# Optimization experiments

Measured on AMD Instinct MI355X. Metric: run time of the kernel, lower is better.

The kernel has to match this reference:

```python
import jax, jax.numpy as jnp
import numpy as np

FACTOR = 8
IN_DIM = 4096
OUT_DIM = 4096


def setup_inputs() -> dict:
    key = jax.random.key(0)
    kx, ka, ks = jax.random.split(key, 3)
    x = jax.random.normal(kx, (4, 2048, IN_DIM), dtype=jnp.float32)
    a = jax.random.normal(ka, (FACTOR, FACTOR, FACTOR), dtype=jnp.float32) * 0.1
    s = jax.random.normal(ks, (FACTOR, OUT_DIM // FACTOR, IN_DIM // FACTOR), dtype=jnp.float32) * 0.05
    return {"x": x, "a": a, "s": s}


def reference(x, a, s):
    f = a.shape[0]
    out_dim = a.shape[1] * s.shape[1]
    in_dim = a.shape[2] * s.shape[2]
    # Batched Kronecker product: (f, a_rows*k, a_cols*p) then sum over batch dim f.
    # weight[a*k + ?, c*p + ?] = sum_b a[b, ar, ac] * s[b, kr, pc]
    p = jnp.einsum('bac,bkp->bakcp', a, s)  # (f, f, out/f, f, in/f)
    weight = p.reshape(f, out_dim, in_dim).sum(axis=0)  # (out, in)
    return x @ weight.T
```

## Files before the change

kernel.cpp:

```cpp
#include <hip/hip_runtime.h>
#include <hip/hip_bf16.h>
#include <stdint.h>

namespace {

constexpr int MTOT = 8192;
constexpr int NTOT = 4096;
constexpr int KTOT = 4096;

constexpr int BM = 256, BN = 256, BK = 32;
constexpr int NT = KTOT / BK;

typedef __attribute__((ext_vector_type(8))) short bf16x8;
typedef __attribute__((ext_vector_type(4))) float f32x4;

__device__ inline unsigned short to_bf16(float f) {
    union { float f; uint32_t u; } v; v.f = f;
    return (unsigned short)((v.u + 0x7FFFu + ((v.u >> 16) & 1u)) >> 16);
}

__global__ __launch_bounds__(256) void convert_x_kernel(const float* __restrict__ x,
                                                        unsigned short* __restrict__ xb) {
    int idx = blockIdx.x * 256 + threadIdx.x;
    const f32x4* xv = reinterpret_cast<const f32x4*>(x);
    f32x4 v0 = xv[2 * idx];
    f32x4 v1 = xv[2 * idx + 1];
    union { bf16x8 v; unsigned short s[8]; } o;
    o.s[0] = to_bf16(v0.x); o.s[1] = to_bf16(v0.y);
    o.s[2] = to_bf16(v0.z); o.s[3] = to_bf16(v0.w);
    o.s[4] = to_bf16(v1.x); o.s[5] = to_bf16(v1.y);
    o.s[6] = to_bf16(v1.z); o.s[7] = to_bf16(v1.w);
    reinterpret_cast<bf16x8*>(xb)[idx] = o.v;
}

__global__ __launch_bounds__(256) void gen_w_kernel(const float* __restrict__ a,
                                                    const float* __restrict__ s,
                                                    unsigned short* __restrict__ w) {
    int idx = blockIdx.x * 256 + threadIdx.x;
    int o  = idx >> 9;
    int i8 = idx & 511;
    int i0 = i8 * 8;
    int obig = o >> 9, orow = o & 511;
    int ibig = i0 >> 9, icol = i0 & 511;

    float acc[8];
#pragma unroll
    for (int j = 0; j < 8; ++j) acc[j] = 0.f;

#pragma unroll
    for (int b = 0; b < 8; ++b) {
        float av = a[b * 64 + obig * 8 + ibig];
        const f32x4* sv = reinterpret_cast<const f32x4*>(s + b * 512 * 512 + orow * 512 + icol);
        f32x4 s0 = sv[0], s1 = sv[1];
        acc[0] += av * s0.x; acc[1] += av * s0.y; acc[2] += av * s0.z; acc[3] += av * s0.w;
        acc[4] += av * s1.x; acc[5] += av * s1.y; acc[6] += av * s1.z; acc[7] += av * s1.w;
    }
    union { bf16x8 v; unsigned short q[8]; } ov;
#pragma unroll
    for (int j = 0; j < 8; ++j) ov.q[j] = to_bf16(acc[j]);
    reinterpret_cast<bf16x8*>(w)[idx] = ov.v;
}

__global__ __launch_bounds__(512, 2)
void gemm_bt_kernel(const unsigned short* __restrict__ A,
                    const unsigned short* __restrict__ B,
                    float* __restrict__ C) {
    __shared__ __align__(16) unsigned short As[4][BM][BK];
    __shared__ __align__(16) unsigned short Bs[4][BN][BK];

    int bid = blockIdx.x;
    int swz = (bid & 7) * 64 + (bid >> 3);
    int bm = swz >> 4;
    int bn = swz & 15;

    int tid  = threadIdx.x;
    int wid  = tid >> 6;
    int lane = tid & 63;
    int wm = wid >> 2, wn = wid & 3;

    int srow  = lane >> 2;
    int sslot = (lane & 3) ^ ((srow >> 1) & 3);
    const unsigned short* ag0 = A + (size_t)(bm * BM + wid * 16 + srow) * KTOT + sslot * 8;
    const unsigned short* ag1 = ag0 + (size_t)128 * KTOT;
    const unsigned short* bg0 = B + (size_t)(bn * BN + wid * 16 + srow) * KTOT + sslot * 8;
    const unsigned short* bg1 = bg0 + (size_t)128 * KTOT;

    int rl    = lane & 15;
    int rslot = (lane >> 4) ^ ((rl >> 1) & 3);

    f32x4 acc[8][4];
#pragma unroll
    for (int m = 0; m < 8; ++m)
#pragma unroll
        for (int n = 0; n < 4; ++n) acc[m][n] = (f32x4)0.f;

    auto STAGE = [&](int s, int k0) {
        __builtin_amdgcn_global_load_lds(
            (const __attribute__((address_space(1))) void*)(ag0 + k0),
            (__attribute__((address_space(3))) void*)&As[s][wid * 16][0], 16, 0, 0);
        __builtin_amdgcn_global_load_lds(
            (const __attribute__((address_space(1))) void*)(ag1 + k0),
            (__attribute__((address_space(3))) void*)&As[s][128 + wid * 16][0], 16, 0, 0);
        __builtin_amdgcn_global_load_lds(
            (const __attribute__((address_space(1))) void*)(bg0 + k0),
            (__attribute__((address_space(3))) void*)&Bs[s][wid * 16][0], 16, 0, 0);
        __builtin_amdgcn_global_load_lds(
            (const __attribute__((address_space(1))) void*)(bg1 + k0),
            (__attribute__((address_space(3))) void*)&Bs[s][128 + wid * 16][0], 16, 0, 0);
    };

    auto BODY = [&](int s) {
        bf16x8 af[8], bf[4];
#pragma unroll
        for (int m = 0; m < 8; ++m)
            af[m] = *reinterpret_cast<const bf16x8*>(&As[s][wm * 128 + m * 16 + rl][rslot * 8]);
#pragma unroll
        for (int n = 0; n < 4; ++n)
            bf[n] = *reinterpret_cast<const bf16x8*>(&Bs[s][wn * 64 + n * 16 + rl][rslot * 8]);
        __builtin_amdgcn_s_setprio(1);
#pragma unroll
        for (int m = 0; m < 8; ++m)
#pragma unroll
            for (int n = 0; n < 4; ++n)
                acc[m][n] = __builtin_amdgcn_mfma_f32_16x16x32_bf16(af[m], bf[n], acc[m][n], 0, 0, 0);
        __builtin_amdgcn_s_setprio(0);
    };

    STAGE(0, 0);
    STAGE(1, BK);
    STAGE(2, 2 * BK);
    asm volatile("s_waitcnt vmcnt(8)" ::: "memory");
    __builtin_amdgcn_s_barrier();
    __builtin_amdgcn_sched_barrier(0);

    for (int t = 0; t < NT - 3; ++t) {
        STAGE((t + 3) & 3, (t + 3) * BK);
        BODY(t & 3);
        asm volatile("s_waitcnt vmcnt(8)" ::: "memory");
        __builtin_amdgcn_s_barrier();
        __builtin_amdgcn_sched_barrier(0);
    }
    BODY((NT - 3) & 3);
    asm volatile("s_waitcnt vmcnt(4)" ::: "memory");
    __builtin_amdgcn_s_barrier();
    __builtin_amdgcn_sched_barrier(0);

    BODY((NT - 2) & 3);
    asm volatile("s_waitcnt vmcnt(0)" ::: "memory");
    __builtin_amdgcn_s_barrier();
    __builtin_amdgcn_sched_barrier(0);

    BODY((NT - 1) & 3);

    int crow0 = bm * BM + wm * 128 + (lane >> 4) * 4;
    int ccol0 = bn * BN + wn * 64 + (lane & 15);
#pragma unroll
    for (int m = 0; m < 8; ++m)
#pragma unroll
        for (int n = 0; n < 4; ++n)
#pragma unroll
            for (int j = 0; j < 4; ++j) {
                size_t r = (size_t)(crow0 + m * 16 + j);
                size_t c = (size_t)(ccol0 + n * 16);
                C[r * NTOT + c] = acc[m][n][j];
            }
}

}

extern "C" void kernel_launch(void* const* d_in, const int* in_sizes, int n_in,
                              void* d_out, int out_size, void* d_ws, size_t ws_size,
                              hipStream_t stream) {
    const float* x = (const float*)d_in[0];
    const float* a = (const float*)d_in[1];
    const float* s = (const float*)d_in[2];
    float* out = (float*)d_out;

    unsigned short* xb = (unsigned short*)d_ws;
    unsigned short* wb = xb + (size_t)MTOT * KTOT;

    convert_x_kernel<<<(MTOT * KTOT / 8) / 256, 256, 0, stream>>>(x, xb);
    gen_w_kernel<<<(NTOT * KTOT / 8) / 256, 256, 0, stream>>>(a, s, wb);
    gemm_bt_kernel<<<(MTOT / 256) * (NTOT / 256), 512, 0, stream>>>(xb, wb, out);
}
```

Baseline: 359.6 us.

## Split GEMM main loop into two interleaved phases with staggered A/B prefetch

Each K-step of the bf16 GEMM is split into two half-phases. Each phase loads part of the fragments from LDS, issues either the A or the B global-to-LDS prefetch, synchronises with extra barriers, and then runs half of the MFMA block. The loop is also unrolled by four so LDS stage indices become compile-time constants. The aim is to interleave LDS reads, global loads and MFMAs more finely across waves, at the cost of more barriers per iteration.

```diff
diff --git a/kernel.cpp b/kernel.cpp
--- a/kernel.cpp
+++ b/kernel.cpp
@@ -94,13 +94,15 @@
 #pragma unroll
         for (int n = 0; n < 4; ++n) acc[m][n] = (f32x4)0.f;
 
-    auto STAGE = [&](int s, int k0) {
+    auto STAGE_A = [&](int s, int k0) {
         __builtin_amdgcn_global_load_lds(
             (const __attribute__((address_space(1))) void*)(ag0 + k0),
             (__attribute__((address_space(3))) void*)&As[s][wid * 16][0], 16, 0, 0);
         __builtin_amdgcn_global_load_lds(
             (const __attribute__((address_space(1))) void*)(ag1 + k0),
             (__attribute__((address_space(3))) void*)&As[s][128 + wid * 16][0], 16, 0, 0);
+    };
+    auto STAGE_B = [&](int s, int k0) {
         __builtin_amdgcn_global_load_lds(
             (const __attribute__((address_space(1))) void*)(bg0 + k0),
             (__attribute__((address_space(3))) void*)&Bs[s][wid * 16][0], 16, 0, 0);
@@ -109,48 +111,78 @@
             (__attribute__((address_space(3))) void*)&Bs[s][128 + wid * 16][0], 16, 0, 0);
     };
 
-    auto BODY = [&](int s) {
-        bf16x8 af[8], bf[4];
-#pragma unroll
-        for (int m = 0; m < 8; ++m)
-            af[m] = *reinterpret_cast<const bf16x8*>(&As[s][wm * 128 + m * 16 + rl][rslot * 8]);
+    bf16x8 bfr[4];
+
+    auto PH0 = [&](int s, bool st, int ss, int k0) {
+        bf16x8 afr[4];
+#pragma unroll
+        for (int m = 0; m < 4; ++m)
+            afr[m] = *reinterpret_cast<const bf16x8*>(&As[s][wm * 128 + m * 16 + rl][rslot * 8]);
 #pragma unroll
         for (int n = 0; n < 4; ++n)
-            bf[n] = *reinterpret_cast<const bf16x8*>(&Bs[s][wn * 64 + n * 16 + rl][rslot * 8]);
+            bfr[n] = *reinterpret_cast<const bf16x8*>(&Bs[s][wn * 64 + n * 16 + rl][rslot * 8]);
+        if (st) STAGE_A(ss, k0);
+        __builtin_amdgcn_s_barrier();
+        asm volatile("s_waitcnt lgkmcnt(0)" ::: "memory");
+        __builtin_amdgcn_sched_barrier(0);
         __builtin_amdgcn_s_setprio(1);
 #pragma unroll
-        for (int m = 0; m < 8; ++m)
+        for (int m = 0; m < 4; ++m)
 #pragma unroll
             for (int n = 0; n < 4; ++n)
-                acc[m][n] = __builtin_amdgcn_mfma_f32_16x16x32_bf16(af[m], bf[n], acc[m][n], 0, 0, 0);
+                acc[m][n] = __builtin_amdgcn_mfma_f32_16x16x32_bf16(afr[m], bfr[n], acc[m][n], 0, 0, 0);
         __builtin_amdgcn_s_setprio(0);
-    };
-
-    STAGE(0, 0);
-    STAGE(1, BK);
-    STAGE(2, 2 * BK);
+        __builtin_amdgcn_s_barrier();
+    };
+    auto PH1 = [&](int s, bool st, int ss, int k0) {
+        bf16x8 afr[4];
+#pragma unroll
+        for (int m = 0; m < 4; ++m)
+            afr[m] = *reinterpret_cast<const bf16x8*>(&As[s][wm * 128 + (m + 4) * 16 + rl][rslot * 8]);
+        if (st) STAGE_B(ss, k0);
+        __builtin_amdgcn_s_barrier();
+        asm volatile("s_waitcnt lgkmcnt(0)" ::: "memory");
+        __builtin_amdgcn_sched_barrier(0);
+        __builtin_amdgcn_s_setprio(1);
+#pragma unroll
+        for (int m = 0; m < 4; ++m)
+#pragma unroll
+            for (int n = 0; n < 4; ++n)
+                acc[m + 4][n] = __builtin_amdgcn_mfma_f32_16x16x32_bf16(afr[m], bfr[n], acc[m + 4][n], 0, 0, 0);
+        __builtin_amdgcn_s_setprio(0);
+    };
+
+    STAGE_A(0, 0);          STAGE_B(0, 0);
+    STAGE_A(1, BK);         STAGE_B(1, BK);
+    STAGE_A(2, 2 * BK);     STAGE_B(2, 2 * BK);
     asm volatile("s_waitcnt vmcnt(8)" ::: "memory");
     __builtin_amdgcn_s_barrier();
-    __builtin_amdgcn_sched_barrier(0);
-
-    for (int t = 0; t < NT - 3; ++t) {
-        STAGE((t + 3) & 3, (t + 3) * BK);
-        BODY(t & 3);
-        asm volatile("s_waitcnt vmcnt(8)" ::: "memory");
-        __builtin_amdgcn_s_barrier();
-        __builtin_amdgcn_sched_barrier(0);
+
+    for (int tb = 0; tb < NT - 4; tb += 4) {
+#pragma unroll
+        for (int u = 0; u < 4; ++u) {
+            int s = u, ss = (u + 3) & 3;
+            int k0 = (tb + u + 3) * BK;
+            PH0(s, true, ss, k0);
+            PH1(s, true, ss, k0);
+            asm volatile("s_waitcnt vmcnt(8)" ::: "memory");
+            __builtin_amdgcn_s_barrier();
+        }
     }
-    BODY((NT - 3) & 3);
+    PH0(0, true, 3, (NT - 1) * BK);
+    PH1(0, true, 3, (NT - 1) * BK);
+    asm volatile("s_waitcnt vmcnt(8)" ::: "memory");
+    __builtin_amdgcn_s_barrier();
+    PH0(1, false, 0, 0);
+    PH1(1, false, 0, 0);
     asm volatile("s_waitcnt vmcnt(4)" ::: "memory");
     __builtin_amdgcn_s_barrier();
-    __builtin_amdgcn_sched_barrier(0);
-
-    BODY((NT - 2) & 3);
+    PH0(2, false, 0, 0);
+    PH1(2, false, 0, 0);
     asm volatile("s_waitcnt vmcnt(0)" ::: "memory");
     __builtin_amdgcn_s_barrier();
-    __builtin_amdgcn_sched_barrier(0);
-
-    BODY((NT - 1) & 3);
+    PH0(3, false, 0, 0);
+    PH1(3, false, 0, 0);
 
     int crow0 = bm * BM + wm * 128 + (lane >> 4) * 4;
     int ccol0 = bn * BN + wn * 64 + (lane & 15);
```

Result: faster. 296.2 us (-17.6%).

## Shrink GEMM tile to 256x128 with 4 waves and triple-buffered LDS

Applied to the files above, without the earlier changes.

Changes the bf16 GEMM block tile from 256x256 with 8 waves to 256x128 with 4 waves, doubling the grid to 1024 blocks. LDS staging drops from 4 buffers to 3, and the main loop is unrolled by 3 so buffer indices are compile-time constants. An explicit lgkmcnt wait now sits before the MFMA block, and several sched_barriers are removed. The aim is to cut LDS per block so two blocks fit per CU and occupancy improves, at the cost of lower per-block data reuse and more global traffic for A.

```diff
diff --git a/kernel.cpp b/kernel.cpp
--- a/kernel.cpp
+++ b/kernel.cpp
@@ -8,7 +8,7 @@
 constexpr int NTOT = 4096;
 constexpr int KTOT = 4096;
 
-constexpr int BM = 256, BN = 256, BK = 32;
+constexpr int BM = 256, BN = 128, BK = 32;
 constexpr int NT = KTOT / BK;
 
 typedef __attribute__((ext_vector_type(8))) short bf16x8;
@@ -61,29 +61,27 @@
     reinterpret_cast<bf16x8*>(w)[idx] = ov.v;
 }
 
-__global__ __launch_bounds__(512, 2)
+__global__ __launch_bounds__(256, 2)
 void gemm_bt_kernel(const unsigned short* __restrict__ A,
                     const unsigned short* __restrict__ B,
                     float* __restrict__ C) {
-    __shared__ __align__(16) unsigned short As[4][BM][BK];
-    __shared__ __align__(16) unsigned short Bs[4][BN][BK];
+    __shared__ __align__(16) unsigned short As[3][BM][BK];
+    __shared__ __align__(16) unsigned short Bs[3][BN][BK];
 
     int bid = blockIdx.x;
-    int swz = (bid & 7) * 64 + (bid >> 3);
-    int bm = swz >> 4;
-    int bn = swz & 15;
+    int swz = (bid & 7) * 128 + (bid >> 3);
+    int bm = swz >> 5;
+    int bn = swz & 31;
 
     int tid  = threadIdx.x;
     int wid  = tid >> 6;
     int lane = tid & 63;
-    int wm = wid >> 2, wn = wid & 3;
+    int wm = wid >> 1, wn = wid & 1;
 
     int srow  = lane >> 2;
     int sslot = (lane & 3) ^ ((srow >> 1) & 3);
-    const unsigned short* ag0 = A + (size_t)(bm * BM + wid * 16 + srow) * KTOT + sslot * 8;
-    const unsigned short* ag1 = ag0 + (size_t)128 * KTOT;
-    const unsigned short* bg0 = B + (size_t)(bn * BN + wid * 16 + srow) * KTOT + sslot * 8;
-    const unsigned short* bg1 = bg0 + (size_t)128 * KTOT;
+    const unsigned short* ag = A + (size_t)(bm * BM + wid * 64 + srow) * KTOT + sslot * 8;
+    const unsigned short* bg = B + (size_t)(bn * BN + wid * 32 + srow) * KTOT + sslot * 8;
 
     int rl    = lane & 15;
     int rslot = (lane >> 4) ^ ((rl >> 1) & 3);
@@ -95,62 +93,56 @@
         for (int n = 0; n < 4; ++n) acc[m][n] = (f32x4)0.f;
 
     auto STAGE = [&](int s, int k0) {
-        __builtin_amdgcn_global_load_lds(
-            (const __attribute__((address_space(1))) void*)(ag0 + k0),
-            (__attribute__((address_space(3))) void*)&As[s][wid * 16][0], 16, 0, 0);
-        __builtin_amdgcn_global_load_lds(
-            (const __attribute__((address_space(1))) void*)(ag1 + k0),
-            (__attribute__((address_space(3))) void*)&As[s][128 + wid * 16][0], 16, 0, 0);
-        __builtin_amdgcn_global_load_lds(
-            (const __attribute__((address_space(1))) void*)(bg0 + k0),
-            (__attribute__((address_space(3))) void*)&Bs[s][wid * 16][0], 16, 0, 0);
-        __builtin_amdgcn_global_load_lds(
-            (const __attribute__((address_space(1))) void*)(bg1 + k0),
-            (__attribute__((address_space(3))) void*)&Bs[s][128 + wid * 16][0], 16, 0, 0);
+#pragma unroll
+        for (int g = 0; g < 4; ++g)
+            __builtin_amdgcn_global_load_lds(
+                (const __attribute__((address_space(1))) void*)(ag + (size_t)g * 16 * KTOT + k0),
+                (__attribute__((address_space(3))) void*)&As[s][wid * 64 + g * 16][0], 16, 0, 0);
+#pragma unroll
+        for (int g = 0; g < 2; ++g)
+            __builtin_amdgcn_global_load_lds(
+                (const __attribute__((address_space(1))) void*)(bg + (size_t)g * 16 * KTOT + k0),
+                (__attribute__((address_space(3))) void*)&Bs[s][wid * 32 + g * 16][0], 16, 0, 0);
     };
 
-    auto BODY = [&](int s) {
-        bf16x8 af[8], bf[4];
+    auto COMPUTE = [&](int s) {
+        bf16x8 fa[8], fb[4];
 #pragma unroll
         for (int m = 0; m < 8; ++m)
-            af[m] = *reinterpret_cast<const bf16x8*>(&As[s][wm * 128 + m * 16 + rl][rslot * 8]);
+            fa[m] = *reinterpret_cast<const bf16x8*>(&As[s][wm * 128 + m * 16 + rl][rslot * 8]);
 #pragma unroll
         for (int n = 0; n < 4; ++n)
-            bf[n] = *reinterpret_cast<const bf16x8*>(&Bs[s][wn * 64 + n * 16 + rl][rslot * 8]);
+            fb[n] = *reinterpret_cast<const bf16x8*>(&Bs[s][wn * 64 + n * 16 + rl][rslot * 8]);
+        asm volatile("s_waitcnt lgkmcnt(0)" ::: "memory");
+        __builtin_amdgcn_sched_barrier(0);
         __builtin_amdgcn_s_setprio(1);
 #pragma unroll
         for (int m = 0; m < 8; ++m)
 #pragma unroll
             for (int n = 0; n < 4; ++n)
-                acc[m][n] = __builtin_amdgcn_mfma_f32_16x16x32_bf16(af[m], bf[n], acc[m][n], 0, 0, 0);
+                acc[m][n] = __builtin_amdgcn_mfma_f32_16x16x32_bf16(fa[m], fb[n], acc[m][n], 0, 0, 0);
         __builtin_amdgcn_s_setprio(0);
     };
 
     STAGE(0, 0);
     STAGE(1, BK);
-    STAGE(2, 2 * BK);
-    asm volatile("s_waitcnt vmcnt(8)" ::: "memory");
+    asm volatile("s_waitcnt vmcnt(6)" ::: "memory");
     __builtin_amdgcn_s_barrier();
-    __builtin_amdgcn_sched_barrier(0);
 
-    for (int t = 0; t < NT - 3; ++t) {
-        STAGE((t + 3) & 3, (t + 3) * BK);
-        BODY(t & 3);
-        asm volatile("s_waitcnt vmcnt(8)" ::: "memory");
-        __builtin_amdgcn_s_barrier();
-        __builtin_amdgcn_sched_barrier(0);
+    for (int tb = 0; tb < NT - 2; tb += 3) {
+#pragma unroll
+        for (int u = 0; u < 3; ++u) {
+            const int t = tb + u;
+            STAGE((u + 2) % 3, (t + 2) * BK);
+            COMPUTE(u);
+            asm volatile("s_waitcnt vmcnt(6)" ::: "memory");
+            __builtin_amdgcn_s_barrier();
+        }
     }
-    BODY((NT - 3) & 3);
-    asm volatile("s_waitcnt vmcnt(4)" ::: "memory");
-    __builtin_amdgcn_s_barrier();
-    __builtin_amdgcn_sched_barrier(0);
-
-    BODY((NT - 2) & 3);
+    COMPUTE(0);
     asm volatile("s_waitcnt vmcnt(0)" ::: "memory");
     __builtin_amdgcn_s_barrier();
-    __builtin_amdgcn_sched_barrier(0);
-
-    BODY((NT - 1) & 3);
+    COMPUTE(1);
 
     int crow0 = bm * BM + wm * 128 + (lane >> 4) * 4;
     int ccol0 = bn * BN + wn * 64 + (lane & 15);
@@ -181,5 +173,5 @@
 
     convert_x_kernel<<<(MTOT * KTOT / 8) / 256, 256, 0, stream>>>(x, xb);
     gen_w_kernel<<<(NTOT * KTOT / 8) / 256, 256, 0, stream>>>(a, s, wb);
-    gemm_bt_kernel<<<(MTOT / 256) * (NTOT / 256), 512, 0, stream>>>(xb, wb, out);
+    gemm_bt_kernel<<<(MTOT / BM) * (NTOT / BN), 256, 0, stream>>>(xb, wb, out);
 }
```

Result: faster. 326.9 us (-9.1%).
